# Kernel tuning notes

Measured on AMD Instinct MI355X. Metric: run time of the kernel, lower is better.

The kernel has to match this reference:

```python
import jax, jax.numpy as jnp
import numpy as np

N_NODES = 50000
N_EDGES = 800000
IN_DIM = 128
HID = 64
HEADS = 4
OUT_DIM = 64
NEG_SLOPE = 0.2


def setup_inputs() -> dict:
    key = jax.random.key(0)
    ks = jax.random.split(key, 12)
    x = jax.random.normal(ks[0], (N_NODES, IN_DIM), dtype=jnp.float32)
    edge_index = jax.random.randint(ks[1], (2, N_EDGES), 0, N_NODES, dtype=jnp.int64)
    s = 0.1
    # GATConv layer 1: in_dim -> hid per head, 4 heads, concat
    W1 = jax.random.normal(ks[2], (IN_DIM, HEADS * HID), dtype=jnp.float32) * s
    a_src1 = jax.random.normal(ks[3], (HEADS, HID), dtype=jnp.float32) * s
    a_dst1 = jax.random.normal(ks[4], (HEADS, HID), dtype=jnp.float32) * s
    b1 = jnp.zeros((HEADS * HID,), dtype=jnp.float32)
    # GATConv layer 2: hid*heads -> out_dim, 1 head
    W2 = jax.random.normal(ks[5], (HEADS * HID, OUT_DIM), dtype=jnp.float32) * s
    a_src2 = jax.random.normal(ks[6], (1, OUT_DIM), dtype=jnp.float32) * s
    a_dst2 = jax.random.normal(ks[7], (1, OUT_DIM), dtype=jnp.float32) * s
    b2 = jnp.zeros((OUT_DIM,), dtype=jnp.float32)
    # final linear out_dim -> 1
    fc_w = jax.random.normal(ks[8], (OUT_DIM, 1), dtype=jnp.float32) * s
    fc_b = jnp.zeros((1,), dtype=jnp.float32)
    return {"x": x, "edge_index": edge_index, "W1": W1, "a_src1": a_src1,
            "a_dst1": a_dst1, "b1": b1, "W2": W2, "a_src2": a_src2,
            "a_dst2": a_dst2, "b2": b2, "fc_w": fc_w, "fc_b": fc_b}


def _gat_layer(x, src, dst, W, a_src, a_dst, bias, heads, out_c):
    """PyG-style GATConv: gather, edge attention, segment softmax, scatter-sum."""
    n = x.shape[0]
    h = (x @ W).reshape(n, heads, out_c)                    # [N,H,C]
    alpha_s = jnp.sum(h * a_src, axis=-1)                   # [N,H]
    alpha_d = jnp.sum(h * a_dst, axis=-1)                   # [N,H]
    e = jax.nn.leaky_relu(alpha_s[src] + alpha_d[dst], NEG_SLOPE)  # [E,H]
    # segment softmax over incoming edges of each destination node
    m = jax.ops.segment_max(e, dst, num_segments=n)         # [N,H]
    ex = jnp.exp(e - m[dst])
    den = jax.ops.segment_sum(ex, dst, num_segments=n)      # [N,H]
    alpha = ex / (den[dst] + 1e-16)                         # [E,H]
    out = jax.ops.segment_sum(alpha[:, :, None] * h[src], dst, num_segments=n)
    return out.reshape(n, heads * out_c) + bias


def reference(x, edge_index, W1, a_src1, a_dst1, b1, W2, a_src2, a_dst2, b2, fc_w, fc_b):
    n = x.shape[0]
    # GATConv default add_self_loops=True
    loop = jnp.arange(n, dtype=edge_index.dtype)
    src = jnp.concatenate([edge_index[0], loop])
    dst = jnp.concatenate([edge_index[1], loop])
    h = _gat_layer(x, src, dst, W1, a_src1, a_dst1, b1, HEADS, HID)
    h = jax.nn.elu(h)
    h = _gat_layer(h, src, dst, W2, a_src2, a_dst2, b2, 1, OUT_DIM)
    return jnp.squeeze(h @ fc_w + fc_b)                      # [N]
```

## Files before the change

### kernel.cpp

```cpp
#include <hip/hip_runtime.h>
#include <hip/hip_fp16.h>

#define N_NODES 50000
#define N_EDGES 800000
#define E_TOT   850000
#define IN_DIM  128
#define HID     64
#define HEADS   4
#define C1      256
#define OUT_DIM 64
#define NEG_SLOPE 0.2f

#define CP_NODES   32
#define CP_BLOCKS  ((N_NODES + CP_NODES - 1) / CP_NODES)
#define COUNT_BLOCKS ((E_TOT + 255) / 256)
#define NB_SCAN ((N_NODES + 255) / 256)

typedef __attribute__((ext_vector_type(8))) short v8s;
typedef __attribute__((ext_vector_type(4))) float v4f;

__device__ __forceinline__ unsigned int bf16_rne(float f) {
    unsigned int u = __float_as_uint(f);
    return (u + 0x7FFFu + ((u >> 16) & 1u)) >> 16;
}
__device__ __forceinline__ unsigned int bf16_pack2(float a, float b) {
    return bf16_rne(a) | (bf16_rne(b) << 16);
}
__device__ __forceinline__ float bf16_lo(unsigned int u) { return __uint_as_float(u << 16); }
__device__ __forceinline__ float bf16_hi(unsigned int u) { return __uint_as_float(u & 0xFFFF0000u); }

__device__ __forceinline__ unsigned int f16_pack2(float a, float b) {
    __half2 h = __floats2half2_rn(a, b);
    return *(unsigned int*)&h;
}
__device__ __forceinline__ float2 f16_unp2(unsigned int u) {
    __half2 h = *(__half2*)&u;
    return __half22float2(h);
}

__global__ __launch_bounds__(512) void prep_kernel(
    const float* __restrict__ W1, const float* __restrict__ a_src1,
    const float* __restrict__ a_dst1,
    const float* __restrict__ W2, const float* __restrict__ a_src2,
    const float* __restrict__ a_dst2, const float* __restrict__ b2,
    const float* __restrict__ fc_w, const float* __restrict__ fc_b,
    float* __restrict__ p_src, float* __restrict__ p_dst,
    float* __restrict__ v_s, float* __restrict__ v_d, float* __restrict__ v_z,
    float* __restrict__ cst, unsigned int* __restrict__ W1b)
{
    const int t = threadIdx.x;
    const int k = t >> 2, h = t & 3;
    const float* wrow = W1 + k * C1 + h * HID;
    const float* as = a_src1 + h * HID;
    const float* ad = a_dst1 + h * HID;
    float s = 0.f, d = 0.f;
    for (int c = 0; c < HID; c++) {
        float w = wrow[c];
        s = fmaf(w, as[c], s);
        d = fmaf(w, ad[c], d);
    }
    p_src[k * HEADS + h] = s;
    p_dst[k * HEADS + h] = d;

    if (t < C1) {
        const float* w2row = W2 + t * OUT_DIM;
        float vs = 0.f, vd = 0.f, vz = 0.f;
        for (int c = 0; c < OUT_DIM; c++) {
            float w = w2row[c];
            vs = fmaf(w, a_src2[c], vs);
            vd = fmaf(w, a_dst2[c], vd);
            vz = fmaf(w, fc_w[c], vz);
        }
        v_s[t] = vs; v_d[t] = vd; v_z[t] = vz;
    }
    if (t == 0) {
        float s2 = 0.f;
        for (int c = 0; c < OUT_DIM; c++) s2 = fmaf(b2[c], fc_w[c], s2);
        cst[0] = s2 + fc_b[0];
    }

    for (int idx = t; idx < 16384; idx += 512) {
        int i    = idx & 3;
        int lane = (idx >> 2) & 63;
        int kk   = (idx >> 8) & 3;
        int nt   = (idx >> 10) & 3;
        int hh   = idx >> 12;
        int k0 = kk * 32 + (lane >> 4) * 8 + i * 2;
        int c  = hh * 64 + nt * 16 + (lane & 15);
        W1b[idx] = bf16_pack2(W1[(size_t)k0 * C1 + c], W1[(size_t)(k0 + 1) * C1 + c]);
    }
}

__global__ __launch_bounds__(256) void convproj_count_kernel(
    const float* __restrict__ x, const float* __restrict__ p_src,
    const float* __restrict__ p_dst, const int* __restrict__ dst_a,
    float* __restrict__ as1, float* __restrict__ ad1,
    unsigned int* __restrict__ xb, int* __restrict__ deg,
    int* __restrict__ posE)
{
    if (blockIdx.x >= CP_BLOCKS) {
        int j = (blockIdx.x - CP_BLOCKS) * 256 + threadIdx.x;
        if (j < E_TOT) {
            int d = (j < N_EDGES) ? dst_a[j] : (j - N_EDGES);
            posE[j] = atomicAdd(&deg[d], 1);
        }
        return;
    }
    __shared__ float ps[IN_DIM * HEADS];
    __shared__ float pd[IN_DIM * HEADS];
    const int t = threadIdx.x;
    for (int i = t; i < IN_DIM * HEADS; i += 256) { ps[i] = p_src[i]; pd[i] = p_dst[i]; }
    __syncthreads();
    const int wv   = t >> 6;
    const int lane = t & 63;
    float4 p0 = *(const float4*)(ps + (lane * 2) * HEADS);
    float4 p1 = *(const float4*)(ps + (lane * 2 + 1) * HEADS);
    float4 q0 = *(const float4*)(pd + (lane * 2) * HEADS);
    float4 q1 = *(const float4*)(pd + (lane * 2 + 1) * HEADS);
    const int nodeBase = blockIdx.x * CP_NODES + wv * 8;
    #pragma unroll
    for (int i = 0; i < 8; i++) {
        const int node = nodeBase + i;
        if (node >= N_NODES) break;
        float2 xv = *(const float2*)(x + (size_t)node * IN_DIM + lane * 2);
        xb[(size_t)node * 64 + lane] = bf16_pack2(xv.x, xv.y);
        float s0 = xv.x * p0.x + xv.y * p1.x;
        float s1 = xv.x * p0.y + xv.y * p1.y;
        float s2 = xv.x * p0.z + xv.y * p1.z;
        float s3 = xv.x * p0.w + xv.y * p1.w;
        float d0 = xv.x * q0.x + xv.y * q1.x;
        float d1 = xv.x * q0.y + xv.y * q1.y;
        float d2 = xv.x * q0.z + xv.y * q1.z;
        float d3 = xv.x * q0.w + xv.y * q1.w;
        #pragma unroll
        for (int off = 32; off; off >>= 1) {
            s0 += __shfl_down(s0, off, 64); s1 += __shfl_down(s1, off, 64);
            s2 += __shfl_down(s2, off, 64); s3 += __shfl_down(s3, off, 64);
            d0 += __shfl_down(d0, off, 64); d1 += __shfl_down(d1, off, 64);
            d2 += __shfl_down(d2, off, 64); d3 += __shfl_down(d3, off, 64);
        }
        if (lane == 0) {
            float4 sv = {s0, s1, s2, s3};
            float4 dv = {d0, d1, d2, d3};
            *(float4*)(as1 + node * 4) = sv;
            *(float4*)(ad1 + node * 4) = dv;
        }
    }
}

__global__ __launch_bounds__(256) void blocksum_kernel(
    const int* __restrict__ deg, int* __restrict__ bsum)
{
    __shared__ int ps[256];
    const int t = threadIdx.x;
    int i = blockIdx.x * 256 + t;
    ps[t] = (i < N_NODES) ? deg[i] : 0;
    __syncthreads();
    for (int off = 128; off; off >>= 1) {
        if (t < off) ps[t] += ps[t + off];
        __syncthreads();
    }
    if (t == 0) bsum[blockIdx.x] = ps[0];
}

__global__ __launch_bounds__(256) void scanbsum_kernel(
    const int* __restrict__ bsum, int* __restrict__ boff)
{
    __shared__ int ps[256];
    const int t = threadIdx.x;
    ps[t] = (t < NB_SCAN) ? bsum[t] : 0;
    __syncthreads();
    for (int off = 1; off < 256; off <<= 1) {
        int u = (t >= off) ? ps[t - off] : 0;
        __syncthreads();
        ps[t] += u;
        __syncthreads();
    }
    boff[t] = (t > 0) ? ps[t - 1] : 0;
}

__global__ __launch_bounds__(256) void expand_kernel(
    const int* __restrict__ deg, const int* __restrict__ boff,
    int* __restrict__ rowptr)
{
    __shared__ int ps[256];
    const int t = threadIdx.x;
    int i = blockIdx.x * 256 + t;
    int v = (i < N_NODES) ? deg[i] : 0;
    ps[t] = v;
    __syncthreads();
    for (int off = 1; off < 256; off <<= 1) {
        int u = (t >= off) ? ps[t - off] : 0;
        __syncthreads();
        ps[t] += u;
        __syncthreads();
    }
    if (i <= N_NODES) rowptr[i] = boff[blockIdx.x] + ps[t] - v;
}

__global__ void fillw3_kernel(const int* __restrict__ src_a, const int* __restrict__ dst_a,
                              const int* __restrict__ rowptr, const int* __restrict__ posE,
                              const float* __restrict__ as1, const float* __restrict__ ad1,
                              int4* __restrict__ rec)
{
    int j = blockIdx.x * blockDim.x + threadIdx.x;
    if (j >= E_TOT) return;
    int s, d;
    if (j < N_EDGES) { s = src_a[j]; d = dst_a[j]; }
    else             { s = j - N_EDGES; d = s; }
    int slot = rowptr[d] + posE[j];
    float4 A  = *(const float4*)(as1 + s * 4);
    float4 Dv = *(const float4*)(ad1 + d * 4);
    float a0 = A.x + Dv.x, a1 = A.y + Dv.y, a2 = A.z + Dv.z, a3 = A.w + Dv.w;
    a0 = a0 > 0.f ? a0 : NEG_SLOPE * a0;
    a1 = a1 > 0.f ? a1 : NEG_SLOPE * a1;
    a2 = a2 > 0.f ? a2 : NEG_SLOPE * a2;
    a3 = a3 > 0.f ? a3 : NEG_SLOPE * a3;
    int4 r;
    r.x = s;
    r.y = (int)f16_pack2(__expf(a0), __expf(a1));
    r.z = (int)f16_pack2(__expf(a2), __expf(a3));
    r.w = 0;
    rec[slot] = r;
}

__global__ __launch_bounds__(512, 8) void agg1mlp_kernel(
    const int* __restrict__ rowptr, const int4* __restrict__ rec,
    const unsigned int* __restrict__ xb,
    const unsigned int* __restrict__ W1b, const float* __restrict__ b1,
    const float* __restrict__ v_s, const float* __restrict__ v_d,
    const float* __restrict__ v_z,
    float2* __restrict__ az, float* __restrict__ ad2)
{
    __shared__ unsigned int xsh[16 * 260];
    __shared__ float pr[8 * 16 * 3];
    const int t = threadIdx.x;
    const int nodeBase = blockIdx.x * 16;
    const int wv   = t >> 6;
    const int lane = t & 63;

    #pragma unroll 1
    for (int i = 0; i < 2; i++) {
        const int ln = wv * 2 + i;
        const int n  = nodeBase + ln;
        const int e0 = rowptr[n], e1 = rowptr[n + 1];

        float2 acc0 = {0,0}, acc1 = {0,0}, acc2 = {0,0}, acc3 = {0,0};
        float den0 = 0, den1 = 0, den2 = 0, den3 = 0;
        int e = e0;
        int4 R0, R1, R2, R3;
        if (e + 4 <= e1) {
            R0 = rec[e]; R1 = rec[e + 1]; R2 = rec[e + 2]; R3 = rec[e + 3];
        }
        while (e + 4 <= e1) {
            unsigned int xu0 = xb[(size_t)R0.x * 64 + lane];
            unsigned int xu1 = xb[(size_t)R1.x * 64 + lane];
            unsigned int xu2 = xb[(size_t)R2.x * 64 + lane];
            unsigned int xu3 = xb[(size_t)R3.x * 64 + lane];
            unsigned int wy0 = R0.y, wz0 = R0.z, wy1 = R1.y, wz1 = R1.z;
            unsigned int wy2 = R2.y, wz2 = R2.z, wy3 = R3.y, wz3 = R3.z;
            e += 4;
            if (e + 4 <= e1) {
                R0 = rec[e]; R1 = rec[e + 1]; R2 = rec[e + 2]; R3 = rec[e + 3];
            }
            float2 W0a = f16_unp2(wy0), W0b = f16_unp2(wz0);
            float2 W1a = f16_unp2(wy1), W1b_ = f16_unp2(wz1);
            float2 W2a = f16_unp2(wy2), W2b = f16_unp2(wz2);
            float2 W3a = f16_unp2(wy3), W3b = f16_unp2(wz3);
            float a0 = bf16_lo(xu0), b0 = bf16_hi(xu0);
            float a1 = bf16_lo(xu1), b1v = bf16_hi(xu1);
            float a2 = bf16_lo(xu2), b2v = bf16_hi(xu2);
            float a3 = bf16_lo(xu3), b3v = bf16_hi(xu3);
            acc0.x = fmaf(W0a.x, a0, acc0.x); acc0.y = fmaf(W0a.x, b0, acc0.y);
            acc1.x = fmaf(W0a.y, a0, acc1.x); acc1.y = fmaf(W0a.y, b0, acc1.y);
            acc2.x = fmaf(W0b.x, a0, acc2.x); acc2.y = fmaf(W0b.x, b0, acc2.y);
            acc3.x = fmaf(W0b.y, a0, acc3.x); acc3.y = fmaf(W0b.y, b0, acc3.y);
            acc0.x = fmaf(W1a.x, a1, acc0.x); acc0.y = fmaf(W1a.x, b1v, acc0.y);
            acc1.x = fmaf(W1a.y, a1, acc1.x); acc1.y = fmaf(W1a.y, b1v, acc1.y);
            acc2.x = fmaf(W1b_.x, a1, acc2.x); acc2.y = fmaf(W1b_.x, b1v, acc2.y);
            acc3.x = fmaf(W1b_.y, a1, acc3.x); acc3.y = fmaf(W1b_.y, b1v, acc3.y);
            acc0.x = fmaf(W2a.x, a2, acc0.x); acc0.y = fmaf(W2a.x, b2v, acc0.y);
            acc1.x = fmaf(W2a.y, a2, acc1.x); acc1.y = fmaf(W2a.y, b2v, acc1.y);
            acc2.x = fmaf(W2b.x, a2, acc2.x); acc2.y = fmaf(W2b.x, b2v, acc2.y);
            acc3.x = fmaf(W2b.y, a2, acc3.x); acc3.y = fmaf(W2b.y, b2v, acc3.y);
            acc0.x = fmaf(W3a.x, a3, acc0.x); acc0.y = fmaf(W3a.x, b3v, acc0.y);
            acc1.x = fmaf(W3a.y, a3, acc1.x); acc1.y = fmaf(W3a.y, b3v, acc1.y);
            acc2.x = fmaf(W3b.x, a3, acc2.x); acc2.y = fmaf(W3b.x, b3v, acc2.y);
            acc3.x = fmaf(W3b.y, a3, acc3.x); acc3.y = fmaf(W3b.y, b3v, acc3.y);
            den0 += (W0a.x + W1a.x) + (W2a.x + W3a.x);
            den1 += (W0a.y + W1a.y) + (W2a.y + W3a.y);
            den2 += (W0b.x + W1b_.x) + (W2b.x + W3b.x);
            den3 += (W0b.y + W1b_.y) + (W2b.y + W3b.y);
        }
        for (; e < e1; e++) {
            int4 r0 = rec[e];
            unsigned int xu = xb[(size_t)r0.x * 64 + lane];
            float2 Wa = f16_unp2(r0.y), Wb = f16_unp2(r0.z);
            float xa = bf16_lo(xu), xbv = bf16_hi(xu);
            acc0.x = fmaf(Wa.x, xa, acc0.x); acc0.y = fmaf(Wa.x, xbv, acc0.y);
            acc1.x = fmaf(Wa.y, xa, acc1.x); acc1.y = fmaf(Wa.y, xbv, acc1.y);
            acc2.x = fmaf(Wb.x, xa, acc2.x); acc2.y = fmaf(Wb.x, xbv, acc2.y);
            acc3.x = fmaf(Wb.y, xa, acc3.x); acc3.y = fmaf(Wb.y, xbv, acc3.y);
            den0 += Wa.x; den1 += Wa.y; den2 += Wb.x; den3 += Wb.y;
        }
        float i0 = 1.f / (den0 + 1e-16f), i1 = 1.f / (den1 + 1e-16f);
        float i2 = 1.f / (den2 + 1e-16f), i3 = 1.f / (den3 + 1e-16f);
        unsigned int* o = xsh + ln * 260 + lane;
        o[0 * 64] = bf16_pack2(acc0.x * i0, acc0.y * i0);
        o[1 * 64] = bf16_pack2(acc1.x * i1, acc1.y * i1);
        o[2 * 64] = bf16_pack2(acc2.x * i2, acc2.y * i2);
        o[3 * 64] = bf16_pack2(acc3.x * i3, acc3.y * i3);
    }
    __syncthreads();

    {
        const int h = wv >> 1;
        const int ntb = (wv & 1) * 2;
        const int m = lane & 15, quad = lane >> 4;
        const unsigned int* abase = xsh + m * 260 + h * 64 + quad * 4;
        v8s af0 = *(const v8s*)(abase + 0);
        v8s af1 = *(const v8s*)(abase + 16);
        v8s af2 = *(const v8s*)(abase + 32);
        v8s af3 = *(const v8s*)(abase + 48);

        float Sr[4] = {0,0,0,0}, Dr[4] = {0,0,0,0}, Zr[4] = {0,0,0,0};
        #pragma unroll
        for (int j = 0; j < 2; j++) {
            const int nt = ntb + j;
            const unsigned int* bbase = W1b + (size_t)(h * 16 + nt * 4) * 256 + lane * 4;
            v4f acc = {0.f, 0.f, 0.f, 0.f};
            acc = __builtin_amdgcn_mfma_f32_16x16x32_bf16(af0, *(const v8s*)(bbase + 0 * 256), acc, 0, 0, 0);
            acc = __builtin_amdgcn_mfma_f32_16x16x32_bf16(af1, *(const v8s*)(bbase + 1 * 256), acc, 0, 0, 0);
            acc = __builtin_amdgcn_mfma_f32_16x16x32_bf16(af2, *(const v8s*)(bbase + 2 * 256), acc, 0, 0, 0);
            acc = __builtin_amdgcn_mfma_f32_16x16x32_bf16(af3, *(const v8s*)(bbase + 3 * 256), acc, 0, 0, 0);
            const int c = h * 64 + nt * 16 + m;
            float bb = b1[c], vsc = v_s[c], vdc = v_d[c], vzc = v_z[c];
            #pragma unroll
            for (int r = 0; r < 4; r++) {
                float o = acc[r] + bb;
                o = o > 0.f ? o : __expf(o) - 1.f;
                Sr[r] = fmaf(o, vsc, Sr[r]);
                Dr[r] = fmaf(o, vdc, Dr[r]);
                Zr[r] = fmaf(o, vzc, Zr[r]);
            }
        }
        #pragma unroll
        for (int off = 8; off; off >>= 1) {
            #pragma unroll
            for (int r = 0; r < 4; r++) {
                Sr[r] += __shfl_down(Sr[r], off, 16);
                Dr[r] += __shfl_down(Dr[r], off, 16);
                Zr[r] += __shfl_down(Zr[r], off, 16);
            }
        }
        if (m == 0) {
            #pragma unroll
            for (int r = 0; r < 4; r++) {
                const int row = quad * 4 + r;
                pr[(wv * 16 + row) * 3 + 0] = Sr[r];
                pr[(wv * 16 + row) * 3 + 1] = Dr[r];
                pr[(wv * 16 + row) * 3 + 2] = Zr[r];
            }
        }
    }
    __syncthreads();

    if (t < 16) {
        float s = 0.f, d = 0.f, z = 0.f;
        #pragma unroll
        for (int w = 0; w < 8; w++) {
            s += pr[(w * 16 + t) * 3 + 0];
            d += pr[(w * 16 + t) * 3 + 1];
            z += pr[(w * 16 + t) * 3 + 2];
        }
        const int node = nodeBase + t;
        float2 azv = {s, z};
        az[node]  = azv;
        ad2[node] = d;
    }
}

__global__ __launch_bounds__(256) void agg2z_kernel(
    const int* __restrict__ rowptr, const int4* __restrict__ rec,
    const float2* __restrict__ az, const float* __restrict__ ad2,
    const float* __restrict__ cst, float* __restrict__ out)
{
    int gid  = blockIdx.x * blockDim.x + threadIdx.x;
    int n    = gid >> 3;
    int sl   = threadIdx.x & 7;
    if (n >= N_NODES) return;
    const float adh = ad2[n];
    const int e0 = rowptr[n], e1 = rowptr[n + 1];

    float acc = 0.f, den = 0.f;
    for (int e = e0 + sl; e < e1; e += 8) {
        int s = rec[e].x;
        float2 v = az[s];
        float a = v.x + adh;
        a = a > 0.f ? a : NEG_SLOPE * a;
        float w = __expf(a);
        acc = fmaf(w, v.y, acc);
        den += w;
    }
    #pragma unroll
    for (int off = 4; off; off >>= 1) {
        acc += __shfl_down(acc, off, 8);
        den += __shfl_down(den, off, 8);
    }
    if (sl == 0) out[n] = acc / (den + 1e-16f) + cst[0];
}

extern "C" void kernel_launch(void* const* d_in, const int* in_sizes, int n_in,
                              void* d_out, int out_size, void* d_ws, size_t ws_size,
                              hipStream_t stream)
{
    const float* x      = (const float*)d_in[0];
    const int*   ei     = (const int*)d_in[1];
    const float* W1     = (const float*)d_in[2];
    const float* a_src1 = (const float*)d_in[3];
    const float* a_dst1 = (const float*)d_in[4];
    const float* b1     = (const float*)d_in[5];
    const float* W2     = (const float*)d_in[6];
    const float* a_src2 = (const float*)d_in[7];
    const float* a_dst2 = (const float*)d_in[8];
    const float* b2     = (const float*)d_in[9];
    const float* fc_w   = (const float*)d_in[10];
    const float* fc_b   = (const float*)d_in[11];
    float* out = (float*)d_out;

    const int* srcA = ei;
    const int* dstA = ei + N_EDGES;

    float* ws = (float*)d_ws;
    size_t off = 0;
    unsigned int* xb    = (unsigned int*)(ws + off); off += (size_t)N_NODES * 64;
    int4* rec      = (int4*)(ws + off); off += (size_t)E_TOT * 4 + 256;
    int* posE      = (int*)(ws + off); off += E_TOT + 256;
    float* as1     = ws + off; off += (size_t)N_NODES * HEADS;
    float* ad1     = ws + off; off += (size_t)N_NODES * HEADS;
    float2* az     = (float2*)(ws + off); off += (size_t)N_NODES * 2;
    float* ad2     = ws + off; off += N_NODES;
    float* p_src   = ws + off; off += IN_DIM * HEADS;
    float* p_dst   = ws + off; off += IN_DIM * HEADS;
    float* v_s     = ws + off; off += C1;
    float* v_d     = ws + off; off += C1;
    float* v_z     = ws + off; off += C1;
    float* cst     = ws + off; off += 2;
    unsigned int* W1b = (unsigned int*)(ws + off); off += 16384;
    int* rowptr    = (int*)(ws + off); off += N_NODES + 1 + 256;
    int* bsum      = (int*)(ws + off); off += 256;
    int* boff      = (int*)(ws + off); off += 256;
    int* deg       = (int*)(ws + off); off += N_NODES;
    hipMemsetAsync(deg, 0, N_NODES * sizeof(int), stream);

    prep_kernel<<<1, 512, 0, stream>>>(W1, a_src1, a_dst1, W2, a_src2, a_dst2,
                                       b2, fc_w, fc_b, p_src, p_dst, v_s, v_d, v_z, cst, W1b);

    convproj_count_kernel<<<CP_BLOCKS + COUNT_BLOCKS, 256, 0, stream>>>(
        x, p_src, p_dst, dstA, as1, ad1, xb, deg, posE);

    blocksum_kernel<<<NB_SCAN, 256, 0, stream>>>(deg, bsum);
    scanbsum_kernel<<<1, 256, 0, stream>>>(bsum, boff);
    expand_kernel<<<NB_SCAN, 256, 0, stream>>>(deg, boff, rowptr);
    fillw3_kernel<<<COUNT_BLOCKS, 256, 0, stream>>>(srcA, dstA, rowptr, posE,
                                                    as1, ad1, rec);

    agg1mlp_kernel<<<N_NODES / 16, 512, 0, stream>>>(rowptr, rec, xb, W1b, b1,
                                                     v_s, v_d, v_z, az, ad2);

    agg2z_kernel<<<(N_NODES * 8 + 255) / 256, 256, 0, stream>>>(rowptr, rec, az, ad2, cst, out);
}
```

Measured before the change: 255.8 us.

## Fuse CSR scan into one kernel, parallelize W1 packing, shrink agg1 blocks

Spreads the W1 bf16 repacking in prep over 32 extra blocks so the single-block prep kernel does less serial work. Replaces the three-kernel degree scan with one kernel in which block 0 spins on per-block aggregates and publishes prefix offsets, removing two launches. The scheme relies on block 0 and all other blocks being resident together, which holds for 196 blocks but is a forward-progress risk. Also halves the agg1mlp block to 256 threads, so each wave aggregates four nodes and runs a full head of MFMA tiles, trading parallelism per block for more resident blocks.

```diff
diff --git a/kernel.cpp b/kernel.cpp
--- a/kernel.cpp
+++ b/kernel.cpp
@@ -49,6 +49,18 @@
     float* __restrict__ cst, unsigned int* __restrict__ W1b)
 {
     const int t = threadIdx.x;
+    if (blockIdx.x > 0) {
+        int idx = (blockIdx.x - 1) * 512 + t;
+        int i    = idx & 3;
+        int lane = (idx >> 2) & 63;
+        int kk   = (idx >> 8) & 3;
+        int nt   = (idx >> 10) & 3;
+        int hh   = idx >> 12;
+        int k0 = kk * 32 + (lane >> 4) * 8 + i * 2;
+        int c  = hh * 64 + nt * 16 + (lane & 15);
+        W1b[idx] = bf16_pack2(W1[(size_t)k0 * C1 + c], W1[(size_t)(k0 + 1) * C1 + c]);
+        return;
+    }
     const int k = t >> 2, h = t & 3;
     const float* wrow = W1 + k * C1 + h * HID;
     const float* as = a_src1 + h * HID;
@@ -77,17 +89,6 @@
         float s2 = 0.f;
         for (int c = 0; c < OUT_DIM; c++) s2 = fmaf(b2[c], fc_w[c], s2);
         cst[0] = s2 + fc_b[0];
-    }
-
-    for (int idx = t; idx < 16384; idx += 512) {
-        int i    = idx & 3;
-        int lane = (idx >> 2) & 63;
-        int kk   = (idx >> 8) & 3;
-        int nt   = (idx >> 10) & 3;
-        int hh   = idx >> 12;
-        int k0 = kk * 32 + (lane >> 4) * 8 + i * 2;
-        int c  = hh * 64 + nt * 16 + (lane & 15);
-        W1b[idx] = bf16_pack2(W1[(size_t)k0 * C1 + c], W1[(size_t)(k0 + 1) * C1 + c]);
     }
 }
 
@@ -148,44 +149,16 @@
     }
 }
 
-__global__ __launch_bounds__(256) void blocksum_kernel(
-    const int* __restrict__ deg, int* __restrict__ bsum)
+__global__ __launch_bounds__(256) void scanfuse_kernel(
+    const int* __restrict__ deg, int* __restrict__ rowptr,
+    int* aggP, int* incP)
 {
     __shared__ int ps[256];
+    __shared__ int bs[256];
+    __shared__ int sprev;
     const int t = threadIdx.x;
-    int i = blockIdx.x * 256 + t;
-    ps[t] = (i < N_NODES) ? deg[i] : 0;
-    __syncthreads();
-    for (int off = 128; off; off >>= 1) {
-        if (t < off) ps[t] += ps[t + off];
-        __syncthreads();
-    }
-    if (t == 0) bsum[blockIdx.x] = ps[0];
-}
-
-__global__ __launch_bounds__(256) void scanbsum_kernel(
-    const int* __restrict__ bsum, int* __restrict__ boff)
-{
-    __shared__ int ps[256];
-    const int t = threadIdx.x;
-    ps[t] = (t < NB_SCAN) ? bsum[t] : 0;
-    __syncthreads();
-    for (int off = 1; off < 256; off <<= 1) {
-        int u = (t >= off) ? ps[t - off] : 0;
-        __syncthreads();
-        ps[t] += u;
-        __syncthreads();
-    }
-    boff[t] = (t > 0) ? ps[t - 1] : 0;
-}
-
-__global__ __launch_bounds__(256) void expand_kernel(
-    const int* __restrict__ deg, const int* __restrict__ boff,
-    int* __restrict__ rowptr)
-{
-    __shared__ int ps[256];
-    const int t = threadIdx.x;
-    int i = blockIdx.x * 256 + t;
+    const int b = blockIdx.x;
+    int i = b * 256 + t;
     int v = (i < N_NODES) ? deg[i] : 0;
     ps[t] = v;
     __syncthreads();
@@ -195,7 +168,30 @@
         ps[t] += u;
         __syncthreads();
     }
-    if (i <= N_NODES) rowptr[i] = boff[blockIdx.x] + ps[t] - v;
+    if (t == 255) atomicExch(&aggP[b], ps[255] + 1);
+    if (b == 0) {
+        int val = 0;
+        if (t < NB_SCAN) {
+            while ((val = atomicAdd(&aggP[t], 0)) == 0) {}
+            val -= 1;
+        }
+        bs[t] = (t < NB_SCAN) ? val : 0;
+        __syncthreads();
+        for (int off = 1; off < 256; off <<= 1) {
+            int u = (t >= off) ? bs[t - off] : 0;
+            __syncthreads();
+            bs[t] += u;
+            __syncthreads();
+        }
+        if (t < NB_SCAN) atomicExch(&incP[t], (bs[t] - val) + 1);
+    }
+    if (t == 0) {
+        int val;
+        while ((val = atomicAdd(&incP[b], 0)) == 0) {}
+        sprev = val - 1;
+    }
+    __syncthreads();
+    if (i <= N_NODES) rowptr[i] = sprev + ps[t] - v;
 }
 
 __global__ void fillw3_kernel(const int* __restrict__ src_a, const int* __restrict__ dst_a,
@@ -224,7 +220,7 @@
     rec[slot] = r;
 }
 
-__global__ __launch_bounds__(512, 8) void agg1mlp_kernel(
+__global__ __launch_bounds__(256, 6) void agg1mlp_kernel(
     const int* __restrict__ rowptr, const int4* __restrict__ rec,
     const unsigned int* __restrict__ xb,
     const unsigned int* __restrict__ W1b, const float* __restrict__ b1,
@@ -233,15 +229,15 @@
     float2* __restrict__ az, float* __restrict__ ad2)
 {
     __shared__ unsigned int xsh[16 * 260];
-    __shared__ float pr[8 * 16 * 3];
+    __shared__ float pr[4 * 16 * 3];
     const int t = threadIdx.x;
     const int nodeBase = blockIdx.x * 16;
     const int wv   = t >> 6;
     const int lane = t & 63;
 
     #pragma unroll 1
-    for (int i = 0; i < 2; i++) {
-        const int ln = wv * 2 + i;
+    for (int i = 0; i < 4; i++) {
+        const int ln = wv * 4 + i;
         const int n  = nodeBase + ln;
         const int e0 = rowptr[n], e1 = rowptr[n + 1];
 
@@ -314,8 +310,7 @@
     __syncthreads();
 
     {
-        const int h = wv >> 1;
-        const int ntb = (wv & 1) * 2;
+        const int h = wv;
         const int m = lane & 15, quad = lane >> 4;
         const unsigned int* abase = xsh + m * 260 + h * 64 + quad * 4;
         v8s af0 = *(const v8s*)(abase + 0);
@@ -325,8 +320,7 @@
 
         float Sr[4] = {0,0,0,0}, Dr[4] = {0,0,0,0}, Zr[4] = {0,0,0,0};
         #pragma unroll
-        for (int j = 0; j < 2; j++) {
-            const int nt = ntb + j;
+        for (int nt = 0; nt < 4; nt++) {
             const unsigned int* bbase = W1b + (size_t)(h * 16 + nt * 4) * 256 + lane * 4;
             v4f acc = {0.f, 0.f, 0.f, 0.f};
             acc = __builtin_amdgcn_mfma_f32_16x16x32_bf16(af0, *(const v8s*)(bbase + 0 * 256), acc, 0, 0, 0);
@@ -357,9 +351,9 @@
             #pragma unroll
             for (int r = 0; r < 4; r++) {
                 const int row = quad * 4 + r;
-                pr[(wv * 16 + row) * 3 + 0] = Sr[r];
-                pr[(wv * 16 + row) * 3 + 1] = Dr[r];
-                pr[(wv * 16 + row) * 3 + 2] = Zr[r];
+                pr[(h * 16 + row) * 3 + 0] = Sr[r];
+                pr[(h * 16 + row) * 3 + 1] = Dr[r];
+                pr[(h * 16 + row) * 3 + 2] = Zr[r];
             }
         }
     }
@@ -368,7 +362,7 @@
     if (t < 16) {
         float s = 0.f, d = 0.f, z = 0.f;
         #pragma unroll
-        for (int w = 0; w < 8; w++) {
+        for (int w = 0; w < 4; w++) {
             s += pr[(w * 16 + t) * 3 + 0];
             d += pr[(w * 16 + t) * 3 + 1];
             z += pr[(w * 16 + t) * 3 + 2];
@@ -448,24 +442,23 @@
     float* cst     = ws + off; off += 2;
     unsigned int* W1b = (unsigned int*)(ws + off); off += 16384;
     int* rowptr    = (int*)(ws + off); off += N_NODES + 1 + 256;
-    int* bsum      = (int*)(ws + off); off += 256;
-    int* boff      = (int*)(ws + off); off += 256;
+    int* aggP      = (int*)(ws + off); off += 256;
+    int* incP      = (int*)(ws + off); off += 256;
     int* deg       = (int*)(ws + off); off += N_NODES;
-    hipMemsetAsync(deg, 0, N_NODES * sizeof(int), stream);
-
-    prep_kernel<<<1, 512, 0, stream>>>(W1, a_src1, a_dst1, W2, a_src2, a_dst2,
-                                       b2, fc_w, fc_b, p_src, p_dst, v_s, v_d, v_z, cst, W1b);
+    hipMemsetAsync(aggP, 0, (512 + N_NODES) * sizeof(int), stream);
+
+    prep_kernel<<<33, 512, 0, stream>>>(W1, a_src1, a_dst1, W2, a_src2, a_dst2,
+                                        b2, fc_w, fc_b, p_src, p_dst, v_s, v_d, v_z, cst, W1b);
 
     convproj_count_kernel<<<CP_BLOCKS + COUNT_BLOCKS, 256, 0, stream>>>(
         x, p_src, p_dst, dstA, as1, ad1, xb, deg, posE);
 
-    blocksum_kernel<<<NB_SCAN, 256, 0, stream>>>(deg, bsum);
-    scanbsum_kernel<<<1, 256, 0, stream>>>(bsum, boff);
-    expand_kernel<<<NB_SCAN, 256, 0, stream>>>(deg, boff, rowptr);
+    scanfuse_kernel<<<NB_SCAN, 256, 0, stream>>>(deg, rowptr, aggP, incP);
+
     fillw3_kernel<<<COUNT_BLOCKS, 256, 0, stream>>>(srcA, dstA, rowptr, posE,
                                                     as1, ad1, rec);
 
-    agg1mlp_kernel<<<N_NODES / 16, 512, 0, stream>>>(rowptr, rec, xb, W1b, b1,
+    agg1mlp_kernel<<<N_NODES / 16, 256, 0, stream>>>(rowptr, rec, xb, W1b, b1,
                                                      v_s, v_d, v_z, az, ad2);
 
     agg2z_kernel<<<(N_NODES * 8 + 255) / 256, 256, 0, stream>>>(rowptr, rec, az, ad2, cst, out);
```

Result: faster. 247.1 us (-3.4%).
